# Kernel tuning notes

Measured on AMD Instinct MI355X. Metric: run time of the kernel, lower is better.

The kernel has to match this reference:

```python
import jax, jax.numpy as jnp
import numpy as np

N = 100000
E = 1600000
IN_C = 128
HID = 32
H1 = 4
OUT_C = 32
H2 = 1
NEG_SLOPE = 0.2


def setup_inputs() -> dict:
    key = jax.random.key(0)
    ks = jax.random.split(key, 12)
    g = 0.1  # glorot-ish scale
    return {
        "x": jax.random.normal(ks[0], (N, IN_C), jnp.float32),
        "edge_index": jax.random.randint(ks[1], (2, E), 0, N, jnp.int64),
        "W1": jax.random.normal(ks[2], (IN_C, H1 * HID), jnp.float32) * g,
        "att_src1": jax.random.normal(ks[3], (H1, HID), jnp.float32) * g,
        "att_dst1": jax.random.normal(ks[4], (H1, HID), jnp.float32) * g,
        "b1": jnp.zeros((H1 * HID,), jnp.float32),
        "W2": jax.random.normal(ks[5], (H1 * HID, H2 * OUT_C), jnp.float32) * g,
        "att_src2": jax.random.normal(ks[6], (H2, OUT_C), jnp.float32) * g,
        "att_dst2": jax.random.normal(ks[7], (H2, OUT_C), jnp.float32) * g,
        "b2": jnp.zeros((H2 * OUT_C,), jnp.float32),
    }


def gat_conv(x, src, dst, W, att_src, att_dst, bias, heads, ch):
    n = x.shape[0]
    h = (x @ W).reshape(n, heads, ch)                      # [N,H,C]
    a_src = jnp.sum(h * att_src, axis=-1)                  # [N,H]
    a_dst = jnp.sum(h * att_dst, axis=-1)                  # [N,H]
    e = jax.nn.leaky_relu(a_src[src] + a_dst[dst], NEG_SLOPE)  # [E,H]
    # segment softmax over destination neighborhoods
    m = jax.ops.segment_max(e, dst, num_segments=n)        # [N,H]
    ex = jnp.exp(e - m[dst])
    denom = jax.ops.segment_sum(ex, dst, num_segments=n)   # [N,H]
    alpha = ex / (denom[dst] + 1e-16)                      # [E,H]
    msg = h[src] * alpha[:, :, None]                       # [E,H,C]
    out = jax.ops.segment_sum(msg, dst, num_segments=n)    # [N,H,C]
    return out.reshape(n, heads * ch) + bias


def reference(x, edge_index, W1, att_src1, att_dst1, b1, W2, att_src2, att_dst2, b2):
    # PyG GATConv add_self_loops=True
    loops = jnp.arange(N, dtype=edge_index.dtype)
    src = jnp.concatenate([edge_index[0], loops])
    dst = jnp.concatenate([edge_index[1], loops])
    # dropout is a no-op at inference
    h = gat_conv(x, src, dst, W1, att_src1, att_dst1, b1, H1, HID)
    h = jax.nn.relu(h)
    out = gat_conv(h, src, dst, W2, att_src2, att_dst2, b2, H2, OUT_C)
    return out
```

## Files before the change

kernel.cpp:

```cpp
#include <hip/hip_runtime.h>
#include <hip/hip_bf16.h>


#define NSLOPE 0.2f
#define GSTRIDE 136
#define NB_MAX 400
#define CHUNK 4096
#define CAP 5632

typedef __attribute__((ext_vector_type(8))) short short8;
typedef __attribute__((ext_vector_type(4))) float floatx4;

__device__ __forceinline__ float leaky(float v) { return v > 0.f ? v : NSLOPE * v; }

__device__ __forceinline__ unsigned short f2bf(float f) {
  __hip_bfloat16 b = __float2bfloat16(f);
  return *reinterpret_cast<unsigned short*>(&b);
}
__device__ __forceinline__ float bf2f(unsigned int u) {
  return __uint_as_float(u << 16);
}
__device__ __forceinline__ unsigned int pack2(float a, float b) {
  return (unsigned int)f2bf(a) | ((unsigned int)f2bf(b) << 16);
}

__global__ __launch_bounds__(256) void zero_kernel(int* __restrict__ bincur, int nb) {
  int i = blockIdx.x * 256 + threadIdx.x;
  if (i < nb) bincur[i] = i * CAP;
}

__global__ __launch_bounds__(256, 2) void fused1_kernel(
    const float* __restrict__ x, const float* __restrict__ W,
    const float* __restrict__ atts, const float* __restrict__ attd,
    unsigned short* __restrict__ h, float* __restrict__ asrc, float* __restrict__ adst,
    int n, int g1blocks,
    const int* __restrict__ ei, int* __restrict__ bincur,
    unsigned int* __restrict__ staging, int E, int ET, int nb) {
  __shared__ __align__(16) unsigned char smem[70656];
  const int tid = threadIdx.x;

  if (blockIdx.x < g1blocks) {
    unsigned short* xs = (unsigned short*)smem;
    unsigned short* wt = (unsigned short*)(smem + 34816);
    float* att_s = (float*)(smem + 69632);
    float* att_d = (float*)(smem + 70144);
    const int row0 = blockIdx.x * 128;

    if (tid < 128) { att_s[tid] = atts[tid]; att_d[tid] = attd[tid]; }

    const float4* w4 = (const float4*)W;
#pragma unroll
    for (int i = 0; i < 16; i++) {
      int idx = tid + i * 256;
      int k = idx >> 5, n0 = (idx & 31) * 4;
      float4 v = w4[idx];
      float vv[4] = {v.x, v.y, v.z, v.w};
#pragma unroll
      for (int jj = 0; jj < 4; jj++) {
        int j = (jj + tid) & 3;
        wt[(n0 + j) * GSTRIDE + k] = f2bf(vv[j]);
      }
    }

    const float4* x4 = (const float4*)x;
#pragma unroll
    for (int i = 0; i < 16; i++) {
      int idx = tid + i * 256;
      int r = idx >> 5, c4 = idx & 31;
      float4 v = make_float4(0.f, 0.f, 0.f, 0.f);
      if (row0 + r < n) v = x4[(size_t)(row0 + r) * 32 + c4];
      unsigned int* p = (unsigned int*)&xs[r * GSTRIDE + c4 * 4];
      p[0] = pack2(v.x, v.y);
      p[1] = pack2(v.z, v.w);
    }
    __syncthreads();

    const int l = tid & 63;
    const int w = tid >> 6;
    const int mrow = l & 15;
    const int q = l >> 4;
    floatx4 acc[2][8];
#pragma unroll
    for (int mt = 0; mt < 2; mt++)
#pragma unroll
      for (int nt = 0; nt < 8; nt++) acc[mt][nt] = (floatx4){0.f, 0.f, 0.f, 0.f};

#pragma unroll
    for (int ks = 0; ks < 4; ks++) {
      const int k0 = ks * 32 + q * 8;
      short8 a0 = *(const short8*)&xs[(w * 32 + mrow) * GSTRIDE + k0];
      short8 a1 = *(const short8*)&xs[(w * 32 + 16 + mrow) * GSTRIDE + k0];
#pragma unroll
      for (int nt = 0; nt < 8; nt++) {
        short8 b = *(const short8*)&wt[(nt * 16 + mrow) * GSTRIDE + k0];
        acc[0][nt] = __builtin_amdgcn_mfma_f32_16x16x32_bf16(a0, b, acc[0][nt], 0, 0, 0);
        acc[1][nt] = __builtin_amdgcn_mfma_f32_16x16x32_bf16(a1, b, acc[1][nt], 0, 0, 0);
      }
    }
    __syncthreads();

#pragma unroll
    for (int mt = 0; mt < 2; mt++)
#pragma unroll
      for (int nt = 0; nt < 8; nt++)
#pragma unroll
        for (int i = 0; i < 4; i++) {
          int r = w * 32 + mt * 16 + q * 4 + i;
          xs[r * GSTRIDE + nt * 16 + mrow] = f2bf(acc[mt][nt][i]);
        }
    __syncthreads();

#pragma unroll
    for (int i = 0; i < 8; i++) {
      int idx = tid + i * 256;
      int r = idx >> 4, c8 = (idx & 15) * 8;
      if (row0 + r < n) {
        unsigned int* p = (unsigned int*)&xs[r * GSTRIDE + c8];
        uint4 v = make_uint4(p[0], p[1], p[2], p[3]);
        *(uint4*)(h + (size_t)(row0 + r) * 128 + c8) = v;
      }
    }

#pragma unroll
    for (int rr = 0; rr < 2; rr++) {
      int row = (tid >> 2) + rr * 64;
      int head = tid & 3;
      float ss = 0.f, sd = 0.f;
#pragma unroll
      for (int c = 0; c < 32; c++) {
        int cr = (c + tid) & 31;
        float hv = bf2f(xs[row * GSTRIDE + head * 32 + cr]);
        ss += hv * att_s[head * 32 + cr];
        sd += hv * att_d[head * 32 + cr];
      }
      if (row0 + row < n) {
        asrc[(size_t)(row0 + row) * 4 + head] = ss;
        adst[(size_t)(row0 + row) * 4 + head] = sd;
      }
    }
  } else {
    int* hist  = (int*)smem;
    int* run   = (int*)(smem + 1600);
    int* rbase = (int*)(smem + 3200);
    const int base = (blockIdx.x - g1blocks) * CHUNK;
    for (int i = tid; i < nb; i += 256) { hist[i] = 0; run[i] = 0; }
    __syncthreads();
    int se[16], de[16];
#pragma unroll
    for (int j = 0; j < 16; j++) {
      int idx = base + j * 256 + tid;
      if (idx < ET) {
        if (idx < E) { se[j] = ei[idx]; de[j] = ei[E + idx]; }
        else         { se[j] = de[j] = idx - E; }
        atomicAdd(&hist[de[j] >> 8], 1);
      } else de[j] = -1;
    }
    __syncthreads();
    for (int i = tid; i < nb; i += 256)
      rbase[i] = hist[i] ? atomicAdd(&bincur[i], hist[i]) : 0;
    __syncthreads();
#pragma unroll
    for (int j = 0; j < 16; j++) {
      if (de[j] >= 0) {
        int b = de[j] >> 8;
        int ofs = atomicAdd(&run[b], 1);
        staging[(size_t)rbase[b] + ofs] =
            (unsigned)se[j] | ((unsigned)(de[j] & 255) << 17);
      }
    }
  }
}

__global__ __launch_bounds__(1024, 8) void g1_kernel(const unsigned int* __restrict__ staging,
                                                     const int* __restrict__ bincur,
                                                     const float* __restrict__ asrc,
                                                     const float* __restrict__ adst,
                                                     const unsigned int* __restrict__ h,
                                                     unsigned short* __restrict__ agg,
                                                     int n) {
  __shared__ int lbucket[CAP];
  __shared__ int cnt[256], cur[256], rbeg[256];
  const int b = blockIdx.x;
  const int t = threadIdx.x;
  const int d0 = b << 8;
  const int nd = min(256, n - d0);
  const int base = b * CAP;
  const int rcnt = bincur[b] - base;

  if (t < 256) cnt[t] = 0;
  __syncthreads();
  for (int j = t; j < rcnt; j += 1024)
    atomicAdd(&cnt[staging[(size_t)base + j] >> 17], 1);
  __syncthreads();
  int v = 0;
  if (t < 256) { v = cnt[t]; cur[t] = v; }
  __syncthreads();
  for (int off = 1; off < 256; off <<= 1) {
    int add = (t < 256 && t >= off) ? cur[t - off] : 0;
    __syncthreads();
    if (t < 256) cur[t] += add;
    __syncthreads();
  }
  if (t < 256) { rbeg[t] = cur[t] - v; cur[t] = cur[t] - v; }
  __syncthreads();
  for (int j = t; j < rcnt; j += 1024) {
    unsigned int r = staging[(size_t)base + j];
    int pos = atomicAdd(&cur[r >> 17], 1);
    lbucket[pos] = (int)(r & 0x1FFFFu);
  }
  __syncthreads();

  const int wv = t >> 6;
  const int lane = t & 63;
  const int g = lane >> 3;
  const int l8 = lane & 7;
  const int head = l8 >> 1;
  for (int dd = wv; dd < nd; dd += 16) {
    const int d = d0 + dd;
    const float ad = adst[(size_t)d * 4 + head];
    const int beg = rbeg[dd];
    const int end = beg + cnt[dd];
    float num[16];
#pragma unroll
    for (int j = 0; j < 16; j++) num[j] = 0.f;
    float den = 0.f;

    int i = beg + g;
    if (i < end) {
      int s = lbucket[i];
      for (;;) {
        float a = asrc[(size_t)s * 4 + head];
        const uint4* hp = (const uint4*)(h + (size_t)s * 64 + l8 * 8);
        uint4 h0 = hp[0];
        uint4 h1v = hp[1];
        int i2 = i + 8;
        int s2 = (i2 < end) ? lbucket[i2] : 0;
        float w = __expf(leaky(a + ad));
        den += w;
        num[0]  += w * bf2f(h0.x & 0xffffu);  num[1]  += w * bf2f(h0.x >> 16);
        num[2]  += w * bf2f(h0.y & 0xffffu);  num[3]  += w * bf2f(h0.y >> 16);
        num[4]  += w * bf2f(h0.z & 0xffffu);  num[5]  += w * bf2f(h0.z >> 16);
        num[6]  += w * bf2f(h0.w & 0xffffu);  num[7]  += w * bf2f(h0.w >> 16);
        num[8]  += w * bf2f(h1v.x & 0xffffu); num[9]  += w * bf2f(h1v.x >> 16);
        num[10] += w * bf2f(h1v.y & 0xffffu); num[11] += w * bf2f(h1v.y >> 16);
        num[12] += w * bf2f(h1v.z & 0xffffu); num[13] += w * bf2f(h1v.z >> 16);
        num[14] += w * bf2f(h1v.w & 0xffffu); num[15] += w * bf2f(h1v.w >> 16);
        if (i2 >= end) break;
        i = i2; s = s2;
      }
    }
#pragma unroll
    for (int j = 0; j < 16; j++) {
      num[j] += __shfl_xor(num[j], 8, 64);
      num[j] += __shfl_xor(num[j], 16, 64);
      num[j] += __shfl_xor(num[j], 32, 64);
    }
    den += __shfl_xor(den, 8, 64);
    den += __shfl_xor(den, 16, 64);
    den += __shfl_xor(den, 32, 64);
    if (g == 0) {
      float inv = 1.f / (den + 1e-16f);
      unsigned short* p = agg + (size_t)d * 128 + l8 * 16;
      uint4 o0, o1;
      o0.x = pack2(num[0] * inv, num[1] * inv);
      o0.y = pack2(num[2] * inv, num[3] * inv);
      o0.z = pack2(num[4] * inv, num[5] * inv);
      o0.w = pack2(num[6] * inv, num[7] * inv);
      o1.x = pack2(num[8] * inv, num[9] * inv);
      o1.y = pack2(num[10] * inv, num[11] * inv);
      o1.z = pack2(num[12] * inv, num[13] * inv);
      o1.w = pack2(num[14] * inv, num[15] * inv);
      *(uint4*)p = o0;
      *(uint4*)(p + 8) = o1;
    }
  }
}

__global__ __launch_bounds__(256, 2) void gemm2_kernel(const unsigned short* __restrict__ agg1,
                                                       const float* __restrict__ b1,
                                                       const float* __restrict__ W,
                                                       const float* __restrict__ atts,
                                                       const float* __restrict__ attd,
                                                       unsigned short* __restrict__ h2,
                                                       float* __restrict__ asrc,
                                                       float* __restrict__ adst, int n) {
  __shared__ __align__(16) unsigned short xs[128 * GSTRIDE];
  __shared__ __align__(16) unsigned short wt[32 * GSTRIDE];
  __shared__ __align__(16) unsigned short hs[128 * 36];
  __shared__ float att_s[32], att_d[32];
  const int tid = threadIdx.x;
  const int row0 = blockIdx.x * 128;

  if (tid < 32) { att_s[tid] = atts[tid]; att_d[tid] = attd[tid]; }

  const float4* w4 = (const float4*)W;
#pragma unroll
  for (int i = 0; i < 4; i++) {
    int idx = tid + i * 256;
    int k = idx >> 3, n0 = (idx & 7) * 4;
    float4 v = w4[idx];
    float vv[4] = {v.x, v.y, v.z, v.w};
#pragma unroll
    for (int jj = 0; jj < 4; jj++) {
      int j = (jj + tid) & 3;
      wt[(n0 + j) * GSTRIDE + k] = f2bf(vv[j]);
    }
  }

  const uint4* a4 = (const uint4*)agg1;
#pragma unroll
  for (int i = 0; i < 8; i++) {
    int idx = tid + i * 256;
    int r = idx >> 4, c8 = (idx & 15) * 8;
    uint4 v = make_uint4(0, 0, 0, 0);
    if (row0 + r < n) v = a4[(size_t)(row0 + r) * 16 + (idx & 15)];
    unsigned int* p = (unsigned int*)&xs[r * GSTRIDE + c8];
    unsigned int vw[4] = {v.x, v.y, v.z, v.w};
#pragma unroll
    for (int j = 0; j < 4; j++) {
      float lo = fmaxf(bf2f(vw[j] & 0xffffu) + b1[c8 + j * 2], 0.f);
      float hi = fmaxf(bf2f(vw[j] >> 16) + b1[c8 + j * 2 + 1], 0.f);
      p[j] = pack2(lo, hi);
    }
  }
  __syncthreads();

  const int l = tid & 63;
  const int w = tid >> 6;
  const int mrow = l & 15;
  const int q = l >> 4;
  floatx4 acc[2][2];
#pragma unroll
  for (int mt = 0; mt < 2; mt++)
#pragma unroll
    for (int nt = 0; nt < 2; nt++) acc[mt][nt] = (floatx4){0.f, 0.f, 0.f, 0.f};

#pragma unroll
  for (int ks = 0; ks < 4; ks++) {
    const int k0 = ks * 32 + q * 8;
    short8 a0 = *(const short8*)&xs[(w * 32 + mrow) * GSTRIDE + k0];
    short8 a1 = *(const short8*)&xs[(w * 32 + 16 + mrow) * GSTRIDE + k0];
#pragma unroll
    for (int nt = 0; nt < 2; nt++) {
      short8 b = *(const short8*)&wt[(nt * 16 + mrow) * GSTRIDE + k0];
      acc[0][nt] = __builtin_amdgcn_mfma_f32_16x16x32_bf16(a0, b, acc[0][nt], 0, 0, 0);
      acc[1][nt] = __builtin_amdgcn_mfma_f32_16x16x32_bf16(a1, b, acc[1][nt], 0, 0, 0);
    }
  }

#pragma unroll
  for (int mt = 0; mt < 2; mt++)
#pragma unroll
    for (int nt = 0; nt < 2; nt++)
#pragma unroll
      for (int i = 0; i < 4; i++) {
        int r = w * 32 + mt * 16 + q * 4 + i;
        hs[r * 36 + nt * 16 + mrow] = f2bf(acc[mt][nt][i]);
      }
  __syncthreads();

#pragma unroll
  for (int i = 0; i < 4; i++) {
    int idx = tid + i * 256;
    int r = idx >> 3, c4 = (idx & 7) * 4;
    if (row0 + r < n) {
      unsigned int* p = (unsigned int*)&hs[r * 36 + c4];
      *(uint2*)(h2 + (size_t)(row0 + r) * 32 + c4) = make_uint2(p[0], p[1]);
    }
  }

  if (tid < 128) {
    int row = tid;
    float ss = 0.f, sd = 0.f;
#pragma unroll
    for (int c = 0; c < 32; c++) {
      int cr = (c + tid) & 31;
      float hv = bf2f(hs[row * 36 + cr]);
      ss += hv * att_s[cr];
      sd += hv * att_d[cr];
    }
    if (row0 + row < n) { asrc[row0 + row] = ss; adst[row0 + row] = sd; }
  }
}

__global__ __launch_bounds__(1024, 8) void g2_kernel(const unsigned int* __restrict__ staging,
                                                     const int* __restrict__ bincur,
                                                     const float* __restrict__ asrc,
                                                     const float* __restrict__ adst,
                                                     const unsigned int* __restrict__ h2,
                                                     const float* __restrict__ b2,
                                                     float* __restrict__ out, int n) {
  __shared__ int lbucket[CAP];
  __shared__ int cnt[256], cur[256], rbeg[256];
  const int b = blockIdx.x;
  const int t = threadIdx.x;
  const int d0 = b << 8;
  const int nd = min(256, n - d0);
  const int base = b * CAP;
  const int rcnt = bincur[b] - base;

  if (t < 256) cnt[t] = 0;
  __syncthreads();
  for (int j = t; j < rcnt; j += 1024)
    atomicAdd(&cnt[staging[(size_t)base + j] >> 17], 1);
  __syncthreads();
  int v = 0;
  if (t < 256) { v = cnt[t]; cur[t] = v; }
  __syncthreads();
  for (int off = 1; off < 256; off <<= 1) {
    int add = (t < 256 && t >= off) ? cur[t - off] : 0;
    __syncthreads();
    if (t < 256) cur[t] += add;
    __syncthreads();
  }
  if (t < 256) { rbeg[t] = cur[t] - v; cur[t] = cur[t] - v; }
  __syncthreads();
  for (int j = t; j < rcnt; j += 1024) {
    unsigned int r = staging[(size_t)base + j];
    int pos = atomicAdd(&cur[r >> 17], 1);
    lbucket[pos] = (int)(r & 0x1FFFFu);
  }
  __syncthreads();

  const int wv = t >> 6;
  const int lane = t & 63;
  const int g = lane >> 3;
  const int l8 = lane & 7;
  for (int dd = wv; dd < nd; dd += 16) {
    const int d = d0 + dd;
    const float ad = adst[d];
    const int beg = rbeg[dd];
    const int end = beg + cnt[dd];
    float num[4];
#pragma unroll
    for (int j = 0; j < 4; j++) num[j] = 0.f;
    float den = 0.f;

    int i = beg + g;
    if (i < end) {
      int s = lbucket[i];
      for (;;) {
        float a = asrc[s];
        uint2 hv = *(const uint2*)(h2 + (size_t)s * 16 + l8 * 2);
        int i2 = i + 8;
        int s2 = (i2 < end) ? lbucket[i2] : 0;
        float w = __expf(leaky(a + ad));
        den += w;
        num[0] += w * bf2f(hv.x & 0xffffu); num[1] += w * bf2f(hv.x >> 16);
        num[2] += w * bf2f(hv.y & 0xffffu); num[3] += w * bf2f(hv.y >> 16);
        if (i2 >= end) break;
        i = i2; s = s2;
      }
    }
#pragma unroll
    for (int j = 0; j < 4; j++) {
      num[j] += __shfl_xor(num[j], 8, 64);
      num[j] += __shfl_xor(num[j], 16, 64);
      num[j] += __shfl_xor(num[j], 32, 64);
    }
    den += __shfl_xor(den, 8, 64);
    den += __shfl_xor(den, 16, 64);
    den += __shfl_xor(den, 32, 64);
    if (g == 0) {
      float inv = 1.f / (den + 1e-16f);
      float4 bb = ((const float4*)b2)[l8];
      *(float4*)(out + (size_t)d * 32 + l8 * 4) =
          make_float4(num[0] * inv + bb.x, num[1] * inv + bb.y,
                      num[2] * inv + bb.z, num[3] * inv + bb.w);
    }
  }
}

extern "C" void kernel_launch(void* const* d_in, const int* in_sizes, int n_in,
                              void* d_out, int out_size, void* d_ws, size_t ws_size,
                              hipStream_t stream) {
  const float* x = (const float*)d_in[0];
  const int* ei = (const int*)d_in[1];
  const float* W1 = (const float*)d_in[2];
  const float* atts1 = (const float*)d_in[3];
  const float* attd1 = (const float*)d_in[4];
  const float* b1 = (const float*)d_in[5];
  const float* W2 = (const float*)d_in[6];
  const float* atts2 = (const float*)d_in[7];
  const float* attd2 = (const float*)d_in[8];
  const float* b2 = (const float*)d_in[9];
  float* out = (float*)d_out;

  const int N = in_sizes[0] / 128;
  const int E = in_sizes[1] / 2;
  const int ET = E + N;
  const int NB = (N + 255) >> 8;
  const int NCH = (ET + CHUNK - 1) / CHUNK;
  const int G1B = (N + 127) / 128;

  float* wsf = (float*)d_ws;
  float* asrc1 = wsf;
  float* adst1 = asrc1 + (size_t)N * 4;
  float* asrc2 = adst1 + (size_t)N * 4;
  float* adst2 = asrc2 + (size_t)N;
  unsigned short* agg1 = (unsigned short*)(adst2 + (size_t)N);
  unsigned short* h1 = agg1 + (size_t)N * 128;
  unsigned short* h2 = h1;
  unsigned int* staging = (unsigned int*)(h1 + (size_t)N * 128);
  int* bincur = (int*)(staging + (size_t)NB * CAP);

  zero_kernel<<<(NB + 255) / 256, 256, 0, stream>>>(bincur, NB);
  fused1_kernel<<<G1B + NCH, 256, 0, stream>>>(x, W1, atts1, attd1, h1, asrc1, adst1,
                                               N, G1B, ei, bincur, staging, E, ET, NB);
  g1_kernel<<<NB, 1024, 0, stream>>>(staging, bincur, asrc1, adst1,
                                     (const unsigned int*)h1, agg1, N);
  gemm2_kernel<<<(N + 127) / 128, 256, 0, stream>>>(agg1, b1, W2, atts2, attd2,
                                                    h2, asrc2, adst2, N);
  g2_kernel<<<NB, 1024, 0, stream>>>(staging, bincur, asrc2, adst2,
                                     (const unsigned int*)h2, b2, out, N);
}
```

Before: 289.2 us.

## Split per-bin CSR build into separate kernel and use fine-grained aggregation blocks

The per-bin local sort of edges by destination, which both aggregation kernels used to redo in shared memory, moves into one binB kernel that writes a global CSR (rowbeg/rowend/bucket) once. The two aggregation kernels become simple one-wave-per-destination kernels with 256-thread blocks over N/4 blocks. Previously each used 1024-thread blocks with large LDS per bin. This removes the duplicated sort and should improve load balance and occupancy, at the cost of an extra kernel launch and a global write and read of the bucket array. The zero kernel is replaced by a memset, with bin base offsets now added at use.

```diff
diff --git a/kernel.cpp b/kernel.cpp
--- a/kernel.cpp
+++ b/kernel.cpp
@@ -22,11 +22,6 @@
 }
 __device__ __forceinline__ unsigned int pack2(float a, float b) {
   return (unsigned int)f2bf(a) | ((unsigned int)f2bf(b) << 16);
-}
-
-__global__ __launch_bounds__(256) void zero_kernel(int* __restrict__ bincur, int nb) {
-  int i = blockIdx.x * 256 + threadIdx.x;
-  if (i < nb) bincur[i] = i * CAP;
 }
 
 __global__ __launch_bounds__(256, 2) void fused1_kernel(
@@ -157,7 +152,7 @@
     }
     __syncthreads();
     for (int i = tid; i < nb; i += 256)
-      rbase[i] = hist[i] ? atomicAdd(&bincur[i], hist[i]) : 0;
+      rbase[i] = hist[i] ? (i * CAP + atomicAdd(&bincur[i], hist[i])) : 0;
     __syncthreads();
 #pragma unroll
     for (int j = 0; j < 16; j++) {
@@ -171,108 +166,115 @@
   }
 }
 
-__global__ __launch_bounds__(1024, 8) void g1_kernel(const unsigned int* __restrict__ staging,
-                                                     const int* __restrict__ bincur,
-                                                     const float* __restrict__ asrc,
-                                                     const float* __restrict__ adst,
-                                                     const unsigned int* __restrict__ h,
-                                                     unsigned short* __restrict__ agg,
-                                                     int n) {
-  __shared__ int lbucket[CAP];
-  __shared__ int cnt[256], cur[256], rbeg[256];
+__global__ __launch_bounds__(256) void binB_kernel(const unsigned int* __restrict__ staging,
+                                                   const int* __restrict__ bincur,
+                                                   int* __restrict__ rowbeg,
+                                                   int* __restrict__ rowend,
+                                                   int* __restrict__ bucket, int n) {
+  __shared__ int cnt[256];
+  __shared__ int cur[256];
   const int b = blockIdx.x;
   const int t = threadIdx.x;
   const int d0 = b << 8;
   const int nd = min(256, n - d0);
   const int base = b * CAP;
-  const int rcnt = bincur[b] - base;
-
-  if (t < 256) cnt[t] = 0;
-  __syncthreads();
-  for (int j = t; j < rcnt; j += 1024)
-    atomicAdd(&cnt[staging[(size_t)base + j] >> 17], 1);
-  __syncthreads();
-  int v = 0;
-  if (t < 256) { v = cnt[t]; cur[t] = v; }
+  const int rcnt = bincur[b];
+  cnt[t] = 0;
+  __syncthreads();
+  for (int j = t; j < rcnt; j += 256) {
+    unsigned int r = staging[(size_t)base + j];
+    atomicAdd(&cnt[r >> 17], 1);
+  }
+  __syncthreads();
+  int v = cnt[t];
+  cur[t] = v;
   __syncthreads();
   for (int off = 1; off < 256; off <<= 1) {
-    int add = (t < 256 && t >= off) ? cur[t - off] : 0;
-    __syncthreads();
-    if (t < 256) cur[t] += add;
-    __syncthreads();
-  }
-  if (t < 256) { rbeg[t] = cur[t] - v; cur[t] = cur[t] - v; }
-  __syncthreads();
-  for (int j = t; j < rcnt; j += 1024) {
+    int add = (t >= off) ? cur[t - off] : 0;
+    __syncthreads();
+    cur[t] += add;
+    __syncthreads();
+  }
+  int start = base + cur[t] - v;
+  if (t < nd) { rowbeg[d0 + t] = start; rowend[d0 + t] = start + v; }
+  __syncthreads();
+  cur[t] = start;
+  __syncthreads();
+  for (int j = t; j < rcnt; j += 256) {
     unsigned int r = staging[(size_t)base + j];
     int pos = atomicAdd(&cur[r >> 17], 1);
-    lbucket[pos] = (int)(r & 0x1FFFFu);
-  }
-  __syncthreads();
-
-  const int wv = t >> 6;
-  const int lane = t & 63;
+    bucket[pos] = (int)(r & 0x1FFFFu);
+  }
+}
+
+__global__ __launch_bounds__(256) void g1_kernel(const int* __restrict__ rowbeg,
+                                                 const int* __restrict__ rowend,
+                                                 const int* __restrict__ bucket,
+                                                 const float* __restrict__ asrc,
+                                                 const float* __restrict__ adst,
+                                                 const unsigned int* __restrict__ h,
+                                                 unsigned short* __restrict__ agg,
+                                                 int n) {
+  const int lane = threadIdx.x & 63;
   const int g = lane >> 3;
   const int l8 = lane & 7;
   const int head = l8 >> 1;
-  for (int dd = wv; dd < nd; dd += 16) {
-    const int d = d0 + dd;
-    const float ad = adst[(size_t)d * 4 + head];
-    const int beg = rbeg[dd];
-    const int end = beg + cnt[dd];
-    float num[16];
-#pragma unroll
-    for (int j = 0; j < 16; j++) num[j] = 0.f;
-    float den = 0.f;
-
-    int i = beg + g;
-    if (i < end) {
-      int s = lbucket[i];
-      for (;;) {
-        float a = asrc[(size_t)s * 4 + head];
-        const uint4* hp = (const uint4*)(h + (size_t)s * 64 + l8 * 8);
-        uint4 h0 = hp[0];
-        uint4 h1v = hp[1];
-        int i2 = i + 8;
-        int s2 = (i2 < end) ? lbucket[i2] : 0;
-        float w = __expf(leaky(a + ad));
-        den += w;
-        num[0]  += w * bf2f(h0.x & 0xffffu);  num[1]  += w * bf2f(h0.x >> 16);
-        num[2]  += w * bf2f(h0.y & 0xffffu);  num[3]  += w * bf2f(h0.y >> 16);
-        num[4]  += w * bf2f(h0.z & 0xffffu);  num[5]  += w * bf2f(h0.z >> 16);
-        num[6]  += w * bf2f(h0.w & 0xffffu);  num[7]  += w * bf2f(h0.w >> 16);
-        num[8]  += w * bf2f(h1v.x & 0xffffu); num[9]  += w * bf2f(h1v.x >> 16);
-        num[10] += w * bf2f(h1v.y & 0xffffu); num[11] += w * bf2f(h1v.y >> 16);
-        num[12] += w * bf2f(h1v.z & 0xffffu); num[13] += w * bf2f(h1v.z >> 16);
-        num[14] += w * bf2f(h1v.w & 0xffffu); num[15] += w * bf2f(h1v.w >> 16);
-        if (i2 >= end) break;
-        i = i2; s = s2;
-      }
-    }
-#pragma unroll
-    for (int j = 0; j < 16; j++) {
-      num[j] += __shfl_xor(num[j], 8, 64);
-      num[j] += __shfl_xor(num[j], 16, 64);
-      num[j] += __shfl_xor(num[j], 32, 64);
-    }
-    den += __shfl_xor(den, 8, 64);
-    den += __shfl_xor(den, 16, 64);
-    den += __shfl_xor(den, 32, 64);
-    if (g == 0) {
-      float inv = 1.f / (den + 1e-16f);
-      unsigned short* p = agg + (size_t)d * 128 + l8 * 16;
-      uint4 o0, o1;
-      o0.x = pack2(num[0] * inv, num[1] * inv);
-      o0.y = pack2(num[2] * inv, num[3] * inv);
-      o0.z = pack2(num[4] * inv, num[5] * inv);
-      o0.w = pack2(num[6] * inv, num[7] * inv);
-      o1.x = pack2(num[8] * inv, num[9] * inv);
-      o1.y = pack2(num[10] * inv, num[11] * inv);
-      o1.z = pack2(num[12] * inv, num[13] * inv);
-      o1.w = pack2(num[14] * inv, num[15] * inv);
-      *(uint4*)p = o0;
-      *(uint4*)(p + 8) = o1;
-    }
+  const int d = blockIdx.x * 4 + (threadIdx.x >> 6);
+  if (d >= n) return;
+  const float ad = adst[(size_t)d * 4 + head];
+  const int beg = rowbeg[d], end = rowend[d];
+  float num[16];
+#pragma unroll
+  for (int j = 0; j < 16; j++) num[j] = 0.f;
+  float den = 0.f;
+
+  int i = beg + g;
+  if (i < end) {
+    int s = bucket[i];
+    for (;;) {
+      float a = asrc[(size_t)s * 4 + head];
+      const uint4* hp = (const uint4*)(h + (size_t)s * 64 + l8 * 8);
+      uint4 h0 = hp[0];
+      uint4 h1v = hp[1];
+      int i2 = i + 8;
+      int s2 = (i2 < end) ? bucket[i2] : 0;
+      float w = __expf(leaky(a + ad));
+      den += w;
+      num[0]  += w * bf2f(h0.x & 0xffffu);  num[1]  += w * bf2f(h0.x >> 16);
+      num[2]  += w * bf2f(h0.y & 0xffffu);  num[3]  += w * bf2f(h0.y >> 16);
+      num[4]  += w * bf2f(h0.z & 0xffffu);  num[5]  += w * bf2f(h0.z >> 16);
+      num[6]  += w * bf2f(h0.w & 0xffffu);  num[7]  += w * bf2f(h0.w >> 16);
+      num[8]  += w * bf2f(h1v.x & 0xffffu); num[9]  += w * bf2f(h1v.x >> 16);
+      num[10] += w * bf2f(h1v.y & 0xffffu); num[11] += w * bf2f(h1v.y >> 16);
+      num[12] += w * bf2f(h1v.z & 0xffffu); num[13] += w * bf2f(h1v.z >> 16);
+      num[14] += w * bf2f(h1v.w & 0xffffu); num[15] += w * bf2f(h1v.w >> 16);
+      if (i2 >= end) break;
+      i = i2; s = s2;
+    }
+  }
+#pragma unroll
+  for (int j = 0; j < 16; j++) {
+    num[j] += __shfl_xor(num[j], 8, 64);
+    num[j] += __shfl_xor(num[j], 16, 64);
+    num[j] += __shfl_xor(num[j], 32, 64);
+  }
+  den += __shfl_xor(den, 8, 64);
+  den += __shfl_xor(den, 16, 64);
+  den += __shfl_xor(den, 32, 64);
+  if (g == 0) {
+    float inv = 1.f / (den + 1e-16f);
+    unsigned short* p = agg + (size_t)d * 128 + l8 * 16;
+    uint4 o0, o1;
+    o0.x = pack2(num[0] * inv, num[1] * inv);
+    o0.y = pack2(num[2] * inv, num[3] * inv);
+    o0.z = pack2(num[4] * inv, num[5] * inv);
+    o0.w = pack2(num[6] * inv, num[7] * inv);
+    o1.x = pack2(num[8] * inv, num[9] * inv);
+    o1.y = pack2(num[10] * inv, num[11] * inv);
+    o1.z = pack2(num[12] * inv, num[13] * inv);
+    o1.w = pack2(num[14] * inv, num[15] * inv);
+    *(uint4*)p = o0;
+    *(uint4*)(p + 8) = o1;
   }
 }
 
@@ -383,91 +385,57 @@
   }
 }
 
-__global__ __launch_bounds__(1024, 8) void g2_kernel(const unsigned int* __restrict__ staging,
-                                                     const int* __restrict__ bincur,
-                                                     const float* __restrict__ asrc,
-                                                     const float* __restrict__ adst,
-                                                     const unsigned int* __restrict__ h2,
-                                                     const float* __restrict__ b2,
-                                                     float* __restrict__ out, int n) {
-  __shared__ int lbucket[CAP];
-  __shared__ int cnt[256], cur[256], rbeg[256];
-  const int b = blockIdx.x;
-  const int t = threadIdx.x;
-  const int d0 = b << 8;
-  const int nd = min(256, n - d0);
-  const int base = b * CAP;
-  const int rcnt = bincur[b] - base;
-
-  if (t < 256) cnt[t] = 0;
-  __syncthreads();
-  for (int j = t; j < rcnt; j += 1024)
-    atomicAdd(&cnt[staging[(size_t)base + j] >> 17], 1);
-  __syncthreads();
-  int v = 0;
-  if (t < 256) { v = cnt[t]; cur[t] = v; }
-  __syncthreads();
-  for (int off = 1; off < 256; off <<= 1) {
-    int add = (t < 256 && t >= off) ? cur[t - off] : 0;
-    __syncthreads();
-    if (t < 256) cur[t] += add;
-    __syncthreads();
-  }
-  if (t < 256) { rbeg[t] = cur[t] - v; cur[t] = cur[t] - v; }
-  __syncthreads();
-  for (int j = t; j < rcnt; j += 1024) {
-    unsigned int r = staging[(size_t)base + j];
-    int pos = atomicAdd(&cur[r >> 17], 1);
-    lbucket[pos] = (int)(r & 0x1FFFFu);
-  }
-  __syncthreads();
-
-  const int wv = t >> 6;
-  const int lane = t & 63;
+__global__ __launch_bounds__(256) void g2_kernel(const int* __restrict__ rowbeg,
+                                                 const int* __restrict__ rowend,
+                                                 const int* __restrict__ bucket,
+                                                 const float* __restrict__ asrc,
+                                                 const float* __restrict__ adst,
+                                                 const unsigned int* __restrict__ h2,
+                                                 const float* __restrict__ b2,
+                                                 float* __restrict__ out, int n) {
+  const int lane = threadIdx.x & 63;
   const int g = lane >> 3;
   const int l8 = lane & 7;
-  for (int dd = wv; dd < nd; dd += 16) {
-    const int d = d0 + dd;
-    const float ad = adst[d];
-    const int beg = rbeg[dd];
-    const int end = beg + cnt[dd];
-    float num[4];
-#pragma unroll
-    for (int j = 0; j < 4; j++) num[j] = 0.f;
-    float den = 0.f;
-
-    int i = beg + g;
-    if (i < end) {
-      int s = lbucket[i];
-      for (;;) {
-        float a = asrc[s];
-        uint2 hv = *(const uint2*)(h2 + (size_t)s * 16 + l8 * 2);
-        int i2 = i + 8;
-        int s2 = (i2 < end) ? lbucket[i2] : 0;
-        float w = __expf(leaky(a + ad));
-        den += w;
-        num[0] += w * bf2f(hv.x & 0xffffu); num[1] += w * bf2f(hv.x >> 16);
-        num[2] += w * bf2f(hv.y & 0xffffu); num[3] += w * bf2f(hv.y >> 16);
-        if (i2 >= end) break;
-        i = i2; s = s2;
-      }
-    }
-#pragma unroll
-    for (int j = 0; j < 4; j++) {
-      num[j] += __shfl_xor(num[j], 8, 64);
-      num[j] += __shfl_xor(num[j], 16, 64);
-      num[j] += __shfl_xor(num[j], 32, 64);
-    }
-    den += __shfl_xor(den, 8, 64);
-    den += __shfl_xor(den, 16, 64);
-    den += __shfl_xor(den, 32, 64);
-    if (g == 0) {
-      float inv = 1.f / (den + 1e-16f);
-      float4 bb = ((const float4*)b2)[l8];
-      *(float4*)(out + (size_t)d * 32 + l8 * 4) =
-          make_float4(num[0] * inv + bb.x, num[1] * inv + bb.y,
-                      num[2] * inv + bb.z, num[3] * inv + bb.w);
-    }
+  const int d = blockIdx.x * 4 + (threadIdx.x >> 6);
+  if (d >= n) return;
+  const float ad = adst[d];
+  const int beg = rowbeg[d], end = rowend[d];
+  float num[4];
+#pragma unroll
+  for (int j = 0; j < 4; j++) num[j] = 0.f;
+  float den = 0.f;
+
+  int i = beg + g;
+  if (i < end) {
+    int s = bucket[i];
+    for (;;) {
+      float a = asrc[s];
+      uint2 hv = *(const uint2*)(h2 + (size_t)s * 16 + l8 * 2);
+      int i2 = i + 8;
+      int s2 = (i2 < end) ? bucket[i2] : 0;
+      float w = __expf(leaky(a + ad));
+      den += w;
+      num[0] += w * bf2f(hv.x & 0xffffu); num[1] += w * bf2f(hv.x >> 16);
+      num[2] += w * bf2f(hv.y & 0xffffu); num[3] += w * bf2f(hv.y >> 16);
+      if (i2 >= end) break;
+      i = i2; s = s2;
+    }
+  }
+#pragma unroll
+  for (int j = 0; j < 4; j++) {
+    num[j] += __shfl_xor(num[j], 8, 64);
+    num[j] += __shfl_xor(num[j], 16, 64);
+    num[j] += __shfl_xor(num[j], 32, 64);
+  }
+  den += __shfl_xor(den, 8, 64);
+  den += __shfl_xor(den, 16, 64);
+  den += __shfl_xor(den, 32, 64);
+  if (g == 0) {
+    float inv = 1.f / (den + 1e-16f);
+    float4 bb = ((const float4*)b2)[l8];
+    *(float4*)(out + (size_t)d * 32 + l8 * 4) =
+        make_float4(num[0] * inv + bb.x, num[1] * inv + bb.y,
+                    num[2] * inv + bb.z, num[3] * inv + bb.w);
   }
 }
 
@@ -501,16 +469,20 @@
   unsigned short* agg1 = (unsigned short*)(adst2 + (size_t)N);
   unsigned short* h1 = agg1 + (size_t)N * 128;
   unsigned short* h2 = h1;
-  unsigned int* staging = (unsigned int*)(h1 + (size_t)N * 128);
+  int* rowbeg = (int*)(h1 + (size_t)N * 128);
+  int* rowend = rowbeg + N;
+  int* bucket = rowend + N;
+  unsigned int* staging = (unsigned int*)(bucket + (size_t)NB * CAP);
   int* bincur = (int*)(staging + (size_t)NB * CAP);
 
-  zero_kernel<<<(NB + 255) / 256, 256, 0, stream>>>(bincur, NB);
+  hipMemsetAsync(bincur, 0, NB * sizeof(int), stream);
   fused1_kernel<<<G1B + NCH, 256, 0, stream>>>(x, W1, atts1, attd1, h1, asrc1, adst1,
                                                N, G1B, ei, bincur, staging, E, ET, NB);
-  g1_kernel<<<NB, 1024, 0, stream>>>(staging, bincur, asrc1, adst1,
-                                     (const unsigned int*)h1, agg1, N);
+  binB_kernel<<<NB, 256, 0, stream>>>(staging, bincur, rowbeg, rowend, bucket, N);
+  g1_kernel<<<(N + 3) / 4, 256, 0, stream>>>(rowbeg, rowend, bucket, asrc1, adst1,
+                                             (const unsigned int*)h1, agg1, N);
   gemm2_kernel<<<(N + 127) / 128, 256, 0, stream>>>(agg1, b1, W2, atts2, attd2,
                                                     h2, asrc2, adst2, N);
-  g2_kernel<<<NB, 1024, 0, stream>>>(staging, bincur, asrc2, adst2,
-                                     (const unsigned int*)h2, b2, out, N);
-}
+  g2_kernel<<<(N + 3) / 4, 256, 0, stream>>>(rowbeg, rowend, bucket, asrc2, adst2,
+                                             (const unsigned int*)h2, b2, out, N);
+}
```

After: 290.0 us. Within noise of the previous version (+0.3%).
